# Kernel optimization log

Hardware: AMD Instinct MI355X
Metric: run time of the kernel (lower is better)

Reference implementation:

```python
import jax, jax.numpy as jnp
import numpy as np

K = 5
THRESHOLD = 0.1


def _l2norm(x, eps=1e-12):
    # matches torch.nn.functional.normalize(dim=-1)
    n = jnp.sqrt(jnp.sum(x * x, axis=-1, keepdims=True))
    return x / jnp.maximum(n, eps)


def setup_inputs() -> dict:
    key = jax.random.key(0)
    ks = jax.random.split(key, 5)
    B, CDD, HIS, L, LVL, H = 32, 5, 50, 32, 2, 256
    return {
        "cdd_repr": jax.random.normal(ks[0], (B, CDD, H), dtype=jnp.float32),
        "his_repr": jax.random.normal(ks[1], (B, HIS, H), dtype=jnp.float32),
        "his_embedding": jax.random.normal(ks[2], (B, HIS, L, LVL, H), dtype=jnp.float32),
        "his_attn_mask": jax.random.randint(ks[3], (B, HIS, L), 0, 2).astype(jnp.int32),
        # xavier-normal-ish init for the selection projection
        "W": jax.random.normal(ks[4], (H, H), dtype=jnp.float32) * np.float32(np.sqrt(2.0 / (H + H))),
        "b": jnp.zeros((H,), dtype=jnp.float32),
    }


def reference(cdd_repr, his_repr, his_embedding, his_attn_mask, W, b):
    # selection projection + L2 normalize
    c = _l2norm(cdd_repr @ W.T + b)           # [B, cdd, H]
    h = _l2norm(his_repr @ W.T + b)           # [B, his, H]
    # news-level attention scores
    attn = jnp.einsum("bcd,bhd->bch", c, h)   # [B, cdd, his]
    # top-k history selection (sorted descending, like torch.topk)
    vals, idx = jax.lax.top_k(attn, K)        # [B, cdd, k]
    # gather top-k history embeddings / masks per (batch, cdd)
    his_activated = jax.vmap(lambda e, i: e[i])(his_embedding, idx)   # [B, cdd, k, L, lvl, H]
    his_mask_activated = jax.vmap(lambda m, i: m[i])(his_attn_mask, idx)  # [B, cdd, k, L]
    # threshold mask + reweight (fused elementwise)
    w = jnp.where(vals < THRESHOLD, jnp.float32(0.0), vals)
    his_activated = his_activated * w[..., None, None, None]
    return his_activated, his_mask_activated
```

## Files before the change

kernel.cpp:

```cpp
#include <hip/hip_runtime.h>
#include <hip/hip_bf16.h>

#define B_    32
#define CDD_  5
#define HIS_  50
#define L_    32
#define LVL_  2
#define H_    256
#define K_    5
#define NCDD  (B_*CDD_)
#define NHIS  (B_*HIS_)
#define NROWS (NCDD + NHIS)
#define SLAB  (L_*LVL_*H_)
#define OUT0  ((size_t)NCDD*K_*SLAB)

__global__ __launch_bounds__(256) void proj_norm_kernel(
    const float* __restrict__ cdd, const float* __restrict__ his,
    const float* __restrict__ Wm, const float* __restrict__ bias,
    float* __restrict__ Y)
{
    __shared__ float xs[4][H_];
    __shared__ float part[4][4];
    __shared__ float inv[4];
    const int t = threadIdx.x;
    const int r0 = blockIdx.x * 4;

    {
        int rr = t >> 6, cc = t & 63;
        int row = r0 + rr;
        const float* src = (row < NCDD) ? (cdd + (size_t)row * H_)
                                        : (his + (size_t)(row - NCDD) * H_);
        ((float4*)xs[rr])[cc] = ((const float4*)src)[cc];
    }
    __syncthreads();

    float a0 = 0.f, a1 = 0.f, a2 = 0.f, a3 = 0.f;
    const float4* wrow = (const float4*)(Wm + (size_t)t * H_);
    #pragma unroll 8
    for (int c = 0; c < H_ / 4; ++c) {
        float4 wv = wrow[c];
        float4 x0 = ((float4*)xs[0])[c];
        float4 x1 = ((float4*)xs[1])[c];
        float4 x2 = ((float4*)xs[2])[c];
        float4 x3 = ((float4*)xs[3])[c];
        a0 += wv.x*x0.x + wv.y*x0.y + wv.z*x0.z + wv.w*x0.w;
        a1 += wv.x*x1.x + wv.y*x1.y + wv.z*x1.z + wv.w*x1.w;
        a2 += wv.x*x2.x + wv.y*x2.y + wv.z*x2.z + wv.w*x2.w;
        a3 += wv.x*x3.x + wv.y*x3.y + wv.z*x3.z + wv.w*x3.w;
    }
    const float bt = bias[t];
    float y0 = a0 + bt, y1 = a1 + bt, y2 = a2 + bt, y3 = a3 + bt;

    const int wave = t >> 6, lane = t & 63;
    float s0 = y0*y0, s1 = y1*y1, s2 = y2*y2, s3 = y3*y3;
    #pragma unroll
    for (int off = 32; off; off >>= 1) {
        s0 += __shfl_down(s0, off);
        s1 += __shfl_down(s1, off);
        s2 += __shfl_down(s2, off);
        s3 += __shfl_down(s3, off);
    }
    if (lane == 0) { part[0][wave] = s0; part[1][wave] = s1;
                     part[2][wave] = s2; part[3][wave] = s3; }
    __syncthreads();
    if (t < 4) {
        float s = part[t][0] + part[t][1] + part[t][2] + part[t][3];
        inv[t] = 1.0f / fmaxf(sqrtf(s), 1e-12f);
    }
    __syncthreads();

    float* yr = Y + (size_t)r0 * H_ + t;
    yr[0 * H_] = y0 * inv[0];
    yr[1 * H_] = y1 * inv[1];
    yr[2 * H_] = y2 * inv[2];
    yr[3 * H_] = y3 * inv[3];
}

__global__ __launch_bounds__(256) void attn_topk_kernel(
    const float* __restrict__ Y, const int* __restrict__ mask,
    int* __restrict__ idx_ws, float* __restrict__ w_ws,
    float* __restrict__ mask_out)
{
    const int bc = blockIdx.x;
    const int b  = bc / CDD_;
    __shared__ float cs[H_];
    __shared__ float scores[HIS_];
    __shared__ int   sidx[K_];
    const int t = threadIdx.x;

    cs[t] = Y[(size_t)bc * H_ + t];
    __syncthreads();

    const int wave = t >> 6, lane = t & 63;
    for (int h = wave; h < HIS_; h += 4) {
        const float4* hv = (const float4*)(Y + (size_t)(NCDD + b * HIS_ + h) * H_);
        float4 x  = hv[lane];
        float4 c4 = ((float4*)cs)[lane];
        float p = x.x*c4.x + x.y*c4.y + x.z*c4.z + x.w*c4.w;
        #pragma unroll
        for (int off = 32; off; off >>= 1) p += __shfl_down(p, off);
        if (lane == 0) scores[h] = p;
    }
    __syncthreads();

    if (t == 0) {
        #pragma unroll
        for (int k = 0; k < K_; ++k) {
            float best = -1e30f; int bi = 0;
            for (int h = 0; h < HIS_; ++h)
                if (scores[h] > best) { best = scores[h]; bi = h; }
            scores[bi] = -1e30f;
            sidx[k] = bi;
            idx_ws[bc * K_ + k] = bi;
            w_ws[bc * K_ + k]   = (best < 0.1f) ? 0.0f : best;
        }
    }
    __syncthreads();

    if (t < K_ * L_) {
        int k = t / L_, l = t % L_;
        mask_out[((size_t)bc * K_ + k) * L_ + l] =
            (float)mask[((size_t)(b * HIS_ + sidx[k])) * L_ + l];
    }
}

__global__ __launch_bounds__(256) void gather_scale_kernel(
    const float* __restrict__ emb, const int* __restrict__ idx_ws,
    const float* __restrict__ w_ws, float* __restrict__ out)
{
    const int gb    = blockIdx.x;
    const int slice = gb & 7;
    const int bck   = gb >> 3;
    const int bc    = bck / K_;
    const int b     = bc / CDD_;
    const int i     = idx_ws[bck];
    const float w   = w_ws[bck];

    const float4* src = (const float4*)(emb + (size_t)(b * HIS_ + i) * SLAB);
    float4*       dst = (float4*)(out + (size_t)bck * SLAB);
    const int base = slice * 512 + threadIdx.x;

    float4 v0 = src[base];
    float4 v1 = src[base + 256];
    v0.x *= w; v0.y *= w; v0.z *= w; v0.w *= w;
    v1.x *= w; v1.y *= w; v1.z *= w; v1.w *= w;
    dst[base]       = v0;
    dst[base + 256] = v1;
}

extern "C" void kernel_launch(void* const* d_in, const int* in_sizes, int n_in,
                              void* d_out, int out_size, void* d_ws, size_t ws_size,
                              hipStream_t stream) {
    const float* cdd  = (const float*)d_in[0];
    const float* his  = (const float*)d_in[1];
    const float* emb  = (const float*)d_in[2];
    const int*   mask = (const int*)  d_in[3];
    const float* Wm   = (const float*)d_in[4];
    const float* bias = (const float*)d_in[5];
    float* out = (float*)d_out;

    float* Y      = (float*)d_ws;
    int*   idx_ws = (int*)  ((char*)d_ws + (size_t)NROWS*H_*4);
    float* w_ws   = (float*)((char*)d_ws + (size_t)NROWS*H_*4 + 800*4);

    proj_norm_kernel<<<NROWS / 4, 256, 0, stream>>>(cdd, his, Wm, bias, Y);
    attn_topk_kernel<<<NCDD, 256, 0, stream>>>(Y, mask, idx_ws, w_ws, out + OUT0);
    gather_scale_kernel<<<NCDD * K_ * 8, 256, 0, stream>>>(emb, idx_ws, w_ws, out);
}
```

Measured before the change: 196.6 us.

## Process eight rows per projection block and use wave-parallel top-k selection

The projection kernel now computes eight rows per block instead of four. It reads the input rows directly from global memory instead of staging them in shared memory, which halves the number of blocks and reuses each W row over more outputs. The top-k step in the attention kernel replaces a serial single-thread scan with a 64-lane wave argmax reduction using shuffles, repeated K times. This trades fewer blocks, and so less parallelism, for more W reuse, and adds register pressure from the eight accumulators. Each thread now issues redundant broadcast global loads for the input rows.

Measured after the change: 220.2 us. 1.12x slower.

```diff
diff --git a/kernel.cpp b/kernel.cpp
--- a/kernel.cpp
+++ b/kernel.cpp
@@ -14,66 +14,71 @@
 #define SLAB  (L_*LVL_*H_)
 #define OUT0  ((size_t)NCDD*K_*SLAB)
 
+#define ROWS_A 8
+
 __global__ __launch_bounds__(256) void proj_norm_kernel(
     const float* __restrict__ cdd, const float* __restrict__ his,
     const float* __restrict__ Wm, const float* __restrict__ bias,
     float* __restrict__ Y)
 {
-    __shared__ float xs[4][H_];
-    __shared__ float part[4][4];
-    __shared__ float inv[4];
+    __shared__ float part[ROWS_A][4];
+    __shared__ float inv[ROWS_A];
     const int t = threadIdx.x;
-    const int r0 = blockIdx.x * 4;
+    const int r0 = blockIdx.x * ROWS_A;
 
-    {
-        int rr = t >> 6, cc = t & 63;
-        int row = r0 + rr;
-        const float* src = (row < NCDD) ? (cdd + (size_t)row * H_)
-                                        : (his + (size_t)(row - NCDD) * H_);
-        ((float4*)xs[rr])[cc] = ((const float4*)src)[cc];
+    const float4* xr[ROWS_A];
+    #pragma unroll
+    for (int r = 0; r < ROWS_A; ++r) {
+        int row = r0 + r;
+        const float* p = (row < NCDD) ? (cdd + (size_t)row * H_)
+                                      : (his + (size_t)(row - NCDD) * H_);
+        xr[r] = (const float4*)p;
+    }
+
+    float acc[ROWS_A];
+    #pragma unroll
+    for (int r = 0; r < ROWS_A; ++r) acc[r] = 0.f;
+
+    const float4* wrow = (const float4*)(Wm + (size_t)t * H_);
+
+    #pragma unroll 4
+    for (int ch = 0; ch < H_ / 8; ++ch) {
+        float4 w0 = wrow[2*ch];
+        float4 w1 = wrow[2*ch + 1];
+        #pragma unroll
+        for (int r = 0; r < ROWS_A; ++r) {
+            float4 xa = xr[r][2*ch];
+            float4 xb = xr[r][2*ch + 1];
+            acc[r] += w0.x*xa.x + w0.y*xa.y + w0.z*xa.z + w0.w*xa.w
+                    + w1.x*xb.x + w1.y*xb.y + w1.z*xb.z + w1.w*xb.w;
+        }
+    }
+
+    const float bt = bias[t];
+    float y[ROWS_A], ss[ROWS_A];
+    #pragma unroll
+    for (int r = 0; r < ROWS_A; ++r) { y[r] = acc[r] + bt; ss[r] = y[r]*y[r]; }
+
+    const int wave = t >> 6, lane = t & 63;
+    #pragma unroll
+    for (int off = 32; off; off >>= 1) {
+        #pragma unroll
+        for (int r = 0; r < ROWS_A; ++r) ss[r] += __shfl_down(ss[r], off);
+    }
+    if (lane == 0) {
+        #pragma unroll
+        for (int r = 0; r < ROWS_A; ++r) part[r][wave] = ss[r];
     }
     __syncthreads();
-
-    float a0 = 0.f, a1 = 0.f, a2 = 0.f, a3 = 0.f;
-    const float4* wrow = (const float4*)(Wm + (size_t)t * H_);
-    #pragma unroll 8
-    for (int c = 0; c < H_ / 4; ++c) {
-        float4 wv = wrow[c];
-        float4 x0 = ((float4*)xs[0])[c];
-        float4 x1 = ((float4*)xs[1])[c];
-        float4 x2 = ((float4*)xs[2])[c];
-        float4 x3 = ((float4*)xs[3])[c];
-        a0 += wv.x*x0.x + wv.y*x0.y + wv.z*x0.z + wv.w*x0.w;
-        a1 += wv.x*x1.x + wv.y*x1.y + wv.z*x1.z + wv.w*x1.w;
-        a2 += wv.x*x2.x + wv.y*x2.y + wv.z*x2.z + wv.w*x2.w;
-        a3 += wv.x*x3.x + wv.y*x3.y + wv.z*x3.z + wv.w*x3.w;
-    }
-    const float bt = bias[t];
-    float y0 = a0 + bt, y1 = a1 + bt, y2 = a2 + bt, y3 = a3 + bt;
-
-    const int wave = t >> 6, lane = t & 63;
-    float s0 = y0*y0, s1 = y1*y1, s2 = y2*y2, s3 = y3*y3;
-    #pragma unroll
-    for (int off = 32; off; off >>= 1) {
-        s0 += __shfl_down(s0, off);
-        s1 += __shfl_down(s1, off);
-        s2 += __shfl_down(s2, off);
-        s3 += __shfl_down(s3, off);
-    }
-    if (lane == 0) { part[0][wave] = s0; part[1][wave] = s1;
-                     part[2][wave] = s2; part[3][wave] = s3; }
-    __syncthreads();
-    if (t < 4) {
+    if (t < ROWS_A) {
         float s = part[t][0] + part[t][1] + part[t][2] + part[t][3];
         inv[t] = 1.0f / fmaxf(sqrtf(s), 1e-12f);
     }
     __syncthreads();
 
-    float* yr = Y + (size_t)r0 * H_ + t;
-    yr[0 * H_] = y0 * inv[0];
-    yr[1 * H_] = y1 * inv[1];
-    yr[2 * H_] = y2 * inv[2];
-    yr[3 * H_] = y3 * inv[3];
+    float* yp = Y + (size_t)r0 * H_ + t;
+    #pragma unroll
+    for (int r = 0; r < ROWS_A; ++r) yp[r * H_] = y[r] * inv[r];
 }
 
 __global__ __launch_bounds__(256) void attn_topk_kernel(
@@ -103,16 +108,23 @@
     }
     __syncthreads();
 
-    if (t == 0) {
+    if (wave == 0) {
+        float v = (lane < HIS_) ? scores[lane] : -1e30f;
         #pragma unroll
         for (int k = 0; k < K_; ++k) {
-            float best = -1e30f; int bi = 0;
-            for (int h = 0; h < HIS_; ++h)
-                if (scores[h] > best) { best = scores[h]; bi = h; }
-            scores[bi] = -1e30f;
-            sidx[k] = bi;
-            idx_ws[bc * K_ + k] = bi;
-            w_ws[bc * K_ + k]   = (best < 0.1f) ? 0.0f : best;
+            float mv = v; int mi = lane;
+            #pragma unroll
+            for (int off = 32; off; off >>= 1) {
+                float ov = __shfl_xor(mv, off);
+                int   oi = __shfl_xor(mi, off);
+                if (ov > mv || (ov == mv && oi < mi)) { mv = ov; mi = oi; }
+            }
+            if (lane == 0) {
+                sidx[k] = mi;
+                idx_ws[bc * K_ + k] = mi;
+                w_ws[bc * K_ + k]   = (mv < 0.1f) ? 0.0f : mv;
+            }
+            if (lane == mi) v = -1e30f;
         }
     }
     __syncthreads();
@@ -163,7 +175,7 @@
     int*   idx_ws = (int*)  ((char*)d_ws + (size_t)NROWS*H_*4);
     float* w_ws   = (float*)((char*)d_ws + (size_t)NROWS*H_*4 + 800*4);
 
-    proj_norm_kernel<<<NROWS / 4, 256, 0, stream>>>(cdd, his, Wm, bias, Y);
+    proj_norm_kernel<<<NROWS / ROWS_A, 256, 0, stream>>>(cdd, his, Wm, bias, Y);
     attn_topk_kernel<<<NCDD, 256, 0, stream>>>(Y, mask, idx_ws, w_ws, out + OUT0);
     gather_scale_kernel<<<NCDD * K_ * 8, 256, 0, stream>>>(emb, idx_ws, w_ws, out);
 }
```
